# Optimization experiments

Measured on AMD Instinct MI355X. Metric: run time of the kernel, lower is better.

## Reference

```python
import jax, jax.numpy as jnp
import numpy as np

EPS = 1e-5

def _bn(x, g, b):
    m = x.mean(axis=0)
    v = x.var(axis=0)  # biased, matches torch BN training normalization
    return g * (x - m) * jax.lax.rsqrt(v + EPS) + b

def _mlp(x, W1, b1, g1, be1, W2, b2, g2, be2):
    h = jax.nn.relu(_bn(x @ W1 + b1, g1, be1))
    return jax.nn.relu(_bn(h @ W2 + b2, g2, be2))

def setup_inputs() -> dict:
    key = jax.random.key(0)
    ks = jax.random.split(key, 12)
    n, e, d, de = 100000, 1600000, 128, 16
    def lin(k, fan_in, fan_out):
        bound = 1.0 / np.sqrt(fan_in)
        k1, k2 = jax.random.split(k)
        W = jax.random.uniform(k1, (fan_in, fan_out), jnp.float32, -bound, bound)
        b = jax.random.uniform(k2, (fan_out,), jnp.float32, -bound, bound)
        return W, b
    msg_W1, msg_b1 = lin(ks[0], 2 * d + de, d)
    msg_W2, msg_b2 = lin(ks[1], d, d)
    upd_W1, upd_b1 = lin(ks[2], 3 * d, d)
    upd_W2, upd_b2 = lin(ks[3], d, d)
    return {
        "h": jax.random.normal(ks[4], (n, d), jnp.float32),
        "edge_index": jax.random.randint(ks[5], (2, e), 0, n, jnp.int64),
        "edge_attr": jax.random.normal(ks[6], (e, de), jnp.float32),
        "msg_W1": msg_W1, "msg_b1": msg_b1,
        "msg_g1": jnp.ones((d,)), "msg_be1": jnp.zeros((d,)),
        "msg_W2": msg_W2, "msg_b2": msg_b2,
        "msg_g2": jnp.ones((d,)), "msg_be2": jnp.zeros((d,)),
        "upd_W1": upd_W1, "upd_b1": upd_b1,
        "upd_g1": jnp.ones((d,)), "upd_be1": jnp.zeros((d,)),
        "upd_W2": upd_W2, "upd_b2": upd_b2,
        "upd_g2": jnp.ones((d,)), "upd_be2": jnp.zeros((d,)),
    }

def reference(h, edge_index, edge_attr,
              msg_W1, msg_b1, msg_g1, msg_be1, msg_W2, msg_b2, msg_g2, msg_be2,
              upd_W1, upd_b1, upd_g1, upd_be1, upd_W2, upd_b2, upd_g2, upd_be2):
    alpha = 0.5
    n = h.shape[0]
    src = edge_index[0]
    dst = edge_index[1]
    h_i = h[src]  # (e, d)
    h_j = h[dst]  # (e, d)
    msg_args = (msg_W1, msg_b1, msg_g1, msg_be1, msg_W2, msg_b2, msg_g2, msg_be2)
    m_st = _mlp(jnp.concatenate([h_i, h_j, edge_attr], axis=-1), *msg_args)
    m_ts = _mlp(jnp.concatenate([h_j, h_i, edge_attr], axis=-1), *msg_args)
    # NOTE: original code scatters both directions by source nodes (faithful)
    a_st = jax.ops.segment_sum(m_st, src, num_segments=n)
    a_ts = jax.ops.segment_sum(m_ts, src, num_segments=n)
    upd_in = jnp.concatenate([h, alpha * a_st, (1.0 - alpha) * a_ts], axis=-1)
    return _mlp(upd_in, upd_W1, upd_b1, upd_g1, upd_be1, upd_W2, upd_b2, upd_g2, upd_be2)
```

## Files before the change

kernel.cpp:

```cpp
#include <hip/hip_runtime.h>

#define EPS_BN 1e-5f

typedef __bf16 bf16x8 __attribute__((ext_vector_type(8)));
typedef float f32x4 __attribute__((ext_vector_type(4)));
typedef unsigned short us8 __attribute__((ext_vector_type(8)));
typedef unsigned short us4 __attribute__((ext_vector_type(4)));
typedef unsigned int u32x4 __attribute__((ext_vector_type(4)));

__device__ __forceinline__ unsigned short f2bf(float x) {
  unsigned u = __builtin_bit_cast(unsigned, x);
  unsigned r = (u + 0x7fffu + ((u >> 16) & 1u)) >> 16;
  return (unsigned short)r;
}
__device__ __forceinline__ unsigned pack2bf(float a, float b) {
  return (unsigned)f2bf(a) | ((unsigned)f2bf(b) << 16);
}
__device__ __forceinline__ unsigned long long pack4bf(float a, float b, float c, float d) {
  return (unsigned long long)pack2bf(a, b) | ((unsigned long long)pack2bf(c, d) << 32);
}
__device__ __forceinline__ float ubf(unsigned short u) {
  return __builtin_bit_cast(float, (unsigned)u << 16);
}

__device__ __forceinline__ int fragidx(int k, int c) {
  int nf = c >> 4, lr = c & 15, ks = k >> 5, lq = (k >> 3) & 3, j = k & 7;
  return ((((nf << 2) + ks) << 6) | (lq << 4) | lr) * 8 + j;
}

__global__ __launch_bounds__(256) void prep_all(
    const float* __restrict__ mW1, const float* __restrict__ mW2,
    const float* __restrict__ uW1, const float* __restrict__ uW2,
    unsigned short* __restrict__ wfrag) {
  int b = blockIdx.x;
  if (b == 7) {
    const float* s7 = mW1 + 256 * 128;
    unsigned short* oc = wfrag + 7L * 16384;
    for (int i = threadIdx.x; i < 2048; i += 256) oc[i] = f2bf(s7[i]);
    return;
  }
  const float* src;
  float sc = 1.f;
  switch (b) {
    case 0: src = mW1; break;
    case 1: src = mW1 + 16384; break;
    case 2: src = mW2; break;
    case 3: src = uW1; break;
    case 4: src = uW1 + 16384; sc = 0.5f; break;
    case 5: src = uW1 + 32768; sc = 0.5f; break;
    default: src = uW2; break;
  }
  unsigned short* oc = wfrag + (long)b * 16384;
  for (int i = threadIdx.x; i < 16384; i += 256) {
    oc[fragidx(i >> 7, i & 127)] = f2bf(src[i] * sc);
  }
}

__global__ __launch_bounds__(256) void hist_kernel(
    const int* __restrict__ SRC, long E, int* __restrict__ counts) {
  long i = (long)blockIdx.x * 256 + threadIdx.x;
  long str = (long)gridDim.x * 256;
  for (; i < E; i += str) atomicAdd(&counts[SRC[i]], 1);
}

__global__ __launch_bounds__(256) void scan1(
    const int* __restrict__ counts, int n, int* __restrict__ tmp,
    int* __restrict__ bsum) {
  __shared__ int sd[256];
  int b = blockIdx.x, tid = threadIdx.x;
  int base = b * 1024 + tid * 4;
  int c[4], t = 0;
  #pragma unroll
  for (int j = 0; j < 4; ++j) {
    int idx = base + j;
    c[j] = (idx < n) ? counts[idx] : 0;
    t += c[j];
  }
  sd[tid] = t;
  __syncthreads();
  for (int off = 1; off < 256; off <<= 1) {
    int v = (tid >= off) ? sd[tid - off] : 0;
    __syncthreads();
    sd[tid] += v;
    __syncthreads();
  }
  int run = sd[tid] - t;
  #pragma unroll
  for (int j = 0; j < 4; ++j) {
    int idx = base + j;
    if (idx < n) tmp[idx] = run;
    run += c[j];
  }
  if (tid == 255) bsum[b] = sd[255];
}

__global__ __launch_bounds__(256) void scan2(int* __restrict__ bsum, int nb) {
  __shared__ int sd[256];
  int tid = threadIdx.x;
  int v = (tid < nb) ? bsum[tid] : 0;
  sd[tid] = v;
  __syncthreads();
  for (int off = 1; off < 256; off <<= 1) {
    int x = (tid >= off) ? sd[tid - off] : 0;
    __syncthreads();
    sd[tid] += x;
    __syncthreads();
  }
  if (tid < nb) bsum[tid] = sd[tid] - v;
}

__global__ __launch_bounds__(256) void scan3(
    const int* __restrict__ tmp, const int* __restrict__ bsum, int n,
    int* __restrict__ cursor) {
  int i = blockIdx.x * 256 + threadIdx.x;
  if (i < n) cursor[i] = tmp[i] + bsum[i >> 10];
}

__global__ __launch_bounds__(256) void permute_edges(
    const int* __restrict__ SRC, const int* __restrict__ DST,
    const float* __restrict__ EA, long E, int* __restrict__ cursor,
    int* __restrict__ sS, int* __restrict__ sD,
    unsigned short* __restrict__ EAb) {
  long i = (long)blockIdx.x * 256 + threadIdx.x;
  long str = (long)gridDim.x * 256;
  for (; i < E; i += str) {
    int s = SRC[i];
    int pos = atomicAdd(&cursor[s], 1);
    sS[pos] = s;
    sD[pos] = DST[i];
    const float4* ep = (const float4*)(EA + i * 16);
    float4 a = ep[0], b = ep[1], c = ep[2], d = ep[3];
    u32x4 lo, hi;
    lo[0] = pack2bf(a.x, a.y); lo[1] = pack2bf(a.z, a.w);
    lo[2] = pack2bf(b.x, b.y); lo[3] = pack2bf(b.z, b.w);
    hi[0] = pack2bf(c.x, c.y); hi[1] = pack2bf(c.z, c.w);
    hi[2] = pack2bf(d.x, d.y); hi[3] = pack2bf(d.z, d.w);
    *(u32x4*)(EAb + (long)pos * 16) = lo;
    *(u32x4*)(EAb + (long)pos * 16 + 8) = hi;
  }
}

__global__ __launch_bounds__(256) void node_mfma_pq(
    const float* __restrict__ h, const unsigned short* __restrict__ WfA,
    unsigned short* __restrict__ pqb, int n) {
  __shared__ unsigned short WT[16384];
  int tid = threadIdx.x;
  int lid = tid & 63, w = tid >> 6, lr = lid & 15, lq = lid >> 4;
  long rbase = (long)blockIdx.x * 64 + 16 * w;
  long r = rbase + lr;
  bool rv = (r < n);
  long rl = rv ? r : 0;
  const us8* WF8 = (const us8*)WT;

  bf16x8 af[4];
  const float* Ar = h + rl * 128;
  #pragma unroll
  for (int ks = 0; ks < 4; ++ks) {
    int e0 = 32 * ks + 8 * lq;
    float4 x = *(const float4*)(Ar + e0);
    float4 y = *(const float4*)(Ar + e0 + 4);
    u32x4 t;
    t[0] = pack2bf(x.x, x.y); t[1] = pack2bf(x.z, x.w);
    t[2] = pack2bf(y.x, y.y); t[3] = pack2bf(y.z, y.w);
    if (!rv) { t[0] = 0; t[1] = 0; t[2] = 0; t[3] = 0; }
    af[ks] = __builtin_bit_cast(bf16x8, t);
  }

  f32x4 accP[8], accQ[8];
  #pragma unroll
  for (int nf = 0; nf < 8; ++nf) {
    accP[nf] = f32x4{0.f, 0.f, 0.f, 0.f};
    accQ[nf] = f32x4{0.f, 0.f, 0.f, 0.f};
  }

  for (int i = tid; i < 2048; i += 256) ((us8*)WT)[i] = ((const us8*)WfA)[i];
  __syncthreads();
  #pragma unroll
  for (int nf = 0; nf < 8; ++nf) {
    #pragma unroll
    for (int ks = 0; ks < 4; ++ks) {
      bf16x8 bf = __builtin_bit_cast(bf16x8, WF8[(nf * 4 + ks) * 64 + lid]);
      accP[nf] = __builtin_amdgcn_mfma_f32_16x16x32_bf16(af[ks], bf, accP[nf], 0, 0, 0);
    }
  }
  __syncthreads();
  for (int i = tid; i < 2048; i += 256) ((us8*)WT)[i] = ((const us8*)(WfA + 16384))[i];
  __syncthreads();
  #pragma unroll
  for (int nf = 0; nf < 8; ++nf) {
    #pragma unroll
    for (int ks = 0; ks < 4; ++ks) {
      bf16x8 bf = __builtin_bit_cast(bf16x8, WF8[(nf * 4 + ks) * 64 + lid]);
      accQ[nf] = __builtin_amdgcn_mfma_f32_16x16x32_bf16(af[ks], bf, accQ[nf], 0, 0, 0);
    }
  }

  #pragma unroll
  for (int nf = 0; nf < 8; ++nf) {
    #pragma unroll
    for (int i = 0; i < 4; ++i) {
      long nd = rbase + 4 * lq + i;
      if (nd < n) {
        int ch = 16 * nf + lr;
        pqb[nd * 256 + ch] = f2bf(accP[nf][i]);
        pqb[nd * 256 + 128 + ch] = f2bf(accQ[nf][i]);
      }
    }
  }
}

template <bool ABF16>
__global__ __launch_bounds__(256) void node_mfma(
    const void* A0, const void* A1, const void* A2,
    const unsigned short* __restrict__ Wf,
    float* __restrict__ C, int n, int dostats,
    float* __restrict__ sum_out, float* __restrict__ ssq_out, int nk) {
  __shared__ unsigned short WT[16384];
  int tid = threadIdx.x;
  int lid = tid & 63, w = tid >> 6, lr = lid & 15, lq = lid >> 4;
  long rbase = (long)blockIdx.x * 64 + 16 * w;

  const void* As[3] = {A0, A1, A2};
  f32x4 acc[8];
  #pragma unroll
  for (int nf = 0; nf < 8; ++nf) acc[nf] = f32x4{0.f, 0.f, 0.f, 0.f};

  long r = rbase + lr;
  bool rv = (r < n);
  long rl = rv ? r : 0;
  const us8* WF8 = (const us8*)WT;

  for (int c = 0; c < nk; ++c) {
    if (c) __syncthreads();
    const us8* src = (const us8*)(Wf + (long)c * 16384);
    for (int i = tid; i < 2048; i += 256) ((us8*)WT)[i] = src[i];
    __syncthreads();

    bf16x8 af[4];
    if (ABF16) {
      const us8* Ar = (const us8*)((const unsigned short*)As[c] + rl * 128);
      #pragma unroll
      for (int ks = 0; ks < 4; ++ks) {
        us8 v = Ar[ks * 4 + lq];
        if (!rv) v = us8{0, 0, 0, 0, 0, 0, 0, 0};
        af[ks] = __builtin_bit_cast(bf16x8, v);
      }
    } else {
      const float* Ar = (const float*)As[c] + rl * 128;
      #pragma unroll
      for (int ks = 0; ks < 4; ++ks) {
        int e0 = 32 * ks + 8 * lq;
        float4 x = *(const float4*)(Ar + e0);
        float4 y = *(const float4*)(Ar + e0 + 4);
        u32x4 t;
        t[0] = pack2bf(x.x, x.y); t[1] = pack2bf(x.z, x.w);
        t[2] = pack2bf(y.x, y.y); t[3] = pack2bf(y.z, y.w);
        if (!rv) { t[0] = 0; t[1] = 0; t[2] = 0; t[3] = 0; }
        af[ks] = __builtin_bit_cast(bf16x8, t);
      }
    }
    #pragma unroll
    for (int nf = 0; nf < 8; ++nf) {
      #pragma unroll
      for (int ks = 0; ks < 4; ++ks) {
        bf16x8 bf = __builtin_bit_cast(bf16x8, WF8[(nf * 4 + ks) * 64 + lid]);
        acc[nf] = __builtin_amdgcn_mfma_f32_16x16x32_bf16(af[ks], bf, acc[nf], 0, 0, 0);
      }
    }
  }

  float lsum[8], lssq[8];
  #pragma unroll
  for (int nf = 0; nf < 8; ++nf) { lsum[nf] = 0.f; lssq[nf] = 0.f; }
  #pragma unroll
  for (int nf = 0; nf < 8; ++nf) {
    #pragma unroll
    for (int i = 0; i < 4; ++i) {
      long nd = rbase + 4 * lq + i;
      if (nd < n) {
        float v = acc[nf][i];
        C[nd * 128 + 16 * nf + lr] = v;
        lsum[nf] += v; lssq[nf] += v * v;
      }
    }
  }
  if (dostats) {
    #pragma unroll
    for (int nf = 0; nf < 8; ++nf) {
      float v0 = lsum[nf]; v0 += __shfl_xor(v0, 16); v0 += __shfl_xor(v0, 32);
      float v1 = lssq[nf]; v1 += __shfl_xor(v1, 16); v1 += __shfl_xor(v1, 32);
      if (lq == 0) {
        atomicAdd(&sum_out[16 * nf + lr], v0);
        atomicAdd(&ssq_out[16 * nf + lr], v1);
      }
    }
  }
}

__global__ __launch_bounds__(256) void msg_stats1b(
    const unsigned short* __restrict__ PQ,
    const unsigned short* __restrict__ EAb, const float* __restrict__ W1e,
    const int* __restrict__ SRC, const int* __restrict__ DST, long E,
    float* __restrict__ stats) {
  __shared__ float Wel[16][128];
  __shared__ float red[32][16];
  int tid = threadIdx.x;
  for (int i = tid; i < 16 * 128; i += 256) ((float*)Wel)[i] = W1e[i];
  for (int i = tid; i < 512; i += 256) ((float*)red)[i] = 0.f;
  __syncthreads();
  int c4 = tid & 31, grp = tid >> 5;
  float4 s_st = {0,0,0,0}, q_st = {0,0,0,0}, s_ts = {0,0,0,0}, q_ts = {0,0,0,0};
  long stride = (long)gridDim.x * 8;
  for (long e = (long)blockIdx.x * 8 + grp; e < E; e += stride) {
    int s = SRC[e], t = DST[e];
    const unsigned short* Rs = PQ + (long)s * 256;
    const unsigned short* Rt = PQ + (long)t * 256;
    us4 Ps = *(const us4*)(Rs + 4 * c4);
    us4 Qs = *(const us4*)(Rs + 128 + 4 * c4);
    us4 Pt = *(const us4*)(Rt + 4 * c4);
    us4 Qt = *(const us4*)(Rt + 128 + 4 * c4);
    us8 evlo = *(const us8*)(EAb + e * 16);
    us8 evhi = *(const us8*)(EAb + e * 16 + 8);
    float rx = 0.f, ry = 0.f, rz = 0.f, rw = 0.f;
    #pragma unroll
    for (int k = 0; k < 16; ++k) {
      float f = (k < 8) ? ubf(evlo[k & 7]) : ubf(evhi[k & 7]);
      const float4 w4 = *(const float4*)&Wel[k][c4 * 4];
      rx = fmaf(f, w4.x, rx); ry = fmaf(f, w4.y, ry);
      rz = fmaf(f, w4.z, rz); rw = fmaf(f, w4.w, rw);
    }
    float zx = ubf(Ps[0]) + ubf(Qt[0]) + rx, zy = ubf(Ps[1]) + ubf(Qt[1]) + ry;
    float zz = ubf(Ps[2]) + ubf(Qt[2]) + rz, zw = ubf(Ps[3]) + ubf(Qt[3]) + rw;
    s_st.x += zx; s_st.y += zy; s_st.z += zz; s_st.w += zw;
    q_st.x += zx * zx; q_st.y += zy * zy; q_st.z += zz * zz; q_st.w += zw * zw;
    float ux = ubf(Pt[0]) + ubf(Qs[0]) + rx, uy = ubf(Pt[1]) + ubf(Qs[1]) + ry;
    float uz = ubf(Pt[2]) + ubf(Qs[2]) + rz, uw = ubf(Pt[3]) + ubf(Qs[3]) + rw;
    s_ts.x += ux; s_ts.y += uy; s_ts.z += uz; s_ts.w += uw;
    q_ts.x += ux * ux; q_ts.y += uy * uy; q_ts.z += uz * uz; q_ts.w += uw * uw;
  }
  atomicAdd(&red[c4][0], s_st.x);  atomicAdd(&red[c4][1], s_st.y);
  atomicAdd(&red[c4][2], s_st.z);  atomicAdd(&red[c4][3], s_st.w);
  atomicAdd(&red[c4][4], q_st.x);  atomicAdd(&red[c4][5], q_st.y);
  atomicAdd(&red[c4][6], q_st.z);  atomicAdd(&red[c4][7], q_st.w);
  atomicAdd(&red[c4][8], s_ts.x);  atomicAdd(&red[c4][9], s_ts.y);
  atomicAdd(&red[c4][10], s_ts.z); atomicAdd(&red[c4][11], s_ts.w);
  atomicAdd(&red[c4][12], q_ts.x); atomicAdd(&red[c4][13], q_ts.y);
  atomicAdd(&red[c4][14], q_ts.z); atomicAdd(&red[c4][15], q_ts.w);
  __syncthreads();
  #pragma unroll
  for (int rep = 0; rep < 2; ++rep) {
    int j = rep * 256 + tid;
    int cc = j >> 4, k = j & 15, group = k >> 2, comp = k & 3;
    atomicAdd(&stats[group * 128 + cc * 4 + comp], red[cc][k]);
  }
}

template <bool SCATTER>
__global__ __launch_bounds__(256) void msg_mfma6(
    const unsigned short* __restrict__ PQ,
    const unsigned short* __restrict__ EAb,
    const unsigned short* __restrict__ Web,
    const unsigned short* __restrict__ W2f,
    const int* __restrict__ SRC, const int* __restrict__ DST, long E,
    const float* __restrict__ sc1, const float* __restrict__ sc2,
    float* __restrict__ stats2,
    float* __restrict__ a_st, float* __restrict__ a_ts) {
  __shared__ unsigned short W2F[16384];
  __shared__ unsigned short Atile[2][32][136];
  __shared__ int sArr[32];

  int tid = threadIdx.x;
  int c4 = tid & 31;
  int slot = tid >> 5;
  int lid = tid & 63, w = tid >> 6, lr = lid & 15, lq = lid >> 4;
  int dir = w >> 1;
  int half = (w & 1) * 16;

  for (int i = tid; i < 2048; i += 256) ((us8*)W2F)[i] = ((const us8*)W2f)[i];
  const us8* W2F8 = (const us8*)W2F;

  us4 wreg[16];
  #pragma unroll
  for (int k = 0; k < 16; ++k) wreg[k] = *(const us4*)(Web + k * 128 + c4 * 4);

  const float4* sc1v = (const float4*)sc1;
  float4 scst = sc1v[c4], shst = sc1v[32 + c4];
  float4 scts = sc1v[64 + c4], shts = sc1v[96 + c4];

  float s2[8], h2[8];
  float ssum[8], sssq[8];
  if constexpr (SCATTER) {
    const float* scd = sc2 + dir * 256;
    #pragma unroll
    for (int nf = 0; nf < 8; ++nf) {
      int ch = 16 * nf + lr;
      s2[nf] = scd[ch]; h2[nf] = scd[128 + ch];
    }
  } else {
    #pragma unroll
    for (int nf = 0; nf < 8; ++nf) { ssum[nf] = 0.f; sssq[nf] = 0.f; }
  }
  float* accOut = dir ? a_ts : a_st;
  __syncthreads();

  for (long tb = (long)blockIdx.x * 32; tb < E; tb += (long)gridDim.x * 32) {
    int nE = (int)(E - tb < 32 ? E - tb : 32);

    #pragma unroll
    for (int rep = 0; rep < 4; ++rep) {
      int er = rep * 8 + slot;
      if (er < nE) {
        long e = tb + er;
        int s = SRC[e], t = DST[e];
        if (SCATTER && c4 == 0) sArr[er] = s;
        const us4* Rs = (const us4*)(PQ + (long)s * 256);
        const us4* Rt = (const us4*)(PQ + (long)t * 256);
        us4 Ps = Rs[c4];
        us4 Qs = Rs[32 + c4];
        us4 Pt = Rt[c4];
        us4 Qt = Rt[32 + c4];
        us8 evlo = *(const us8*)(EAb + e * 16);
        us8 evhi = *(const us8*)(EAb + e * 16 + 8);
        float rx = 0.f, ry = 0.f, rz = 0.f, rw = 0.f;
        #pragma unroll
        for (int k = 0; k < 16; ++k) {
          float f = (k < 8) ? ubf(evlo[k & 7]) : ubf(evhi[k & 7]);
          rx = fmaf(f, ubf(wreg[k][0]), rx);
          ry = fmaf(f, ubf(wreg[k][1]), ry);
          rz = fmaf(f, ubf(wreg[k][2]), rz);
          rw = fmaf(f, ubf(wreg[k][3]), rw);
        }
        float ax = fmaxf(fmaf(ubf(Ps[0]) + ubf(Qt[0]) + rx, scst.x, shst.x), 0.f);
        float ay = fmaxf(fmaf(ubf(Ps[1]) + ubf(Qt[1]) + ry, scst.y, shst.y), 0.f);
        float az = fmaxf(fmaf(ubf(Ps[2]) + ubf(Qt[2]) + rz, scst.z, shst.z), 0.f);
        float aw = fmaxf(fmaf(ubf(Ps[3]) + ubf(Qt[3]) + rw, scst.w, shst.w), 0.f);
        *(unsigned long long*)&Atile[0][er][c4 * 4] = pack4bf(ax, ay, az, aw);
        float bx = fmaxf(fmaf(ubf(Pt[0]) + ubf(Qs[0]) + rx, scts.x, shts.x), 0.f);
        float by = fmaxf(fmaf(ubf(Pt[1]) + ubf(Qs[1]) + ry, scts.y, shts.y), 0.f);
        float bz = fmaxf(fmaf(ubf(Pt[2]) + ubf(Qs[2]) + rz, scts.z, shts.z), 0.f);
        float bw = fmaxf(fmaf(ubf(Pt[3]) + ubf(Qs[3]) + rw, scts.w, shts.w), 0.f);
        *(unsigned long long*)&Atile[1][er][c4 * 4] = pack4bf(bx, by, bz, bw);
      } else {
        *(unsigned long long*)&Atile[0][er][c4 * 4] = 0ull;
        *(unsigned long long*)&Atile[1][er][c4 * 4] = 0ull;
      }
    }
    __syncthreads();

    int arow = half + lr;
    const char* ap = (const char*)&Atile[dir][arow][0];
    int acolb = lq * 16;
    bf16x8 af[4];
    #pragma unroll
    for (int ks = 0; ks < 4; ++ks) {
      af[ks] = *(const bf16x8*)(ap + ks * 64 + acolb);
    }
    int srow[4];
    if constexpr (SCATTER) {
      #pragma unroll
      for (int i = 0; i < 4; ++i) {
        int row = half + 4 * lq + i;
        srow[i] = (row < nE) ? sArr[row] : -1;
      }
    }
    #pragma unroll
    for (int nf = 0; nf < 8; ++nf) {
      f32x4 acc = {0.f, 0.f, 0.f, 0.f};
      #pragma unroll
      for (int ks = 0; ks < 4; ++ks) {
        bf16x8 bf = __builtin_bit_cast(bf16x8, W2F8[(nf * 4 + ks) * 64 + lid]);
        acc = __builtin_amdgcn_mfma_f32_16x16x32_bf16(af[ks], bf, acc, 0, 0, 0);
      }
      if constexpr (SCATTER) {
        int ch = 16 * nf + lr;
        int cur = srow[0];
        float m = fmaxf(fmaf(acc[0], s2[nf], h2[nf]), 0.f);
        #pragma unroll
        for (int i = 1; i < 4; ++i) {
          float v = fmaxf(fmaf(acc[i], s2[nf], h2[nf]), 0.f);
          if (srow[i] == cur) {
            m += v;
          } else {
            if (cur >= 0 && m != 0.f) atomicAdd(&accOut[(long)cur * 128 + ch], m);
            cur = srow[i]; m = v;
          }
        }
        if (cur >= 0 && m != 0.f) atomicAdd(&accOut[(long)cur * 128 + ch], m);
      } else {
        #pragma unroll
        for (int i = 0; i < 4; ++i) {
          ssum[nf] += acc[i]; sssq[nf] += acc[i] * acc[i];
        }
      }
    }
    __syncthreads();
  }

  if constexpr (!SCATTER) {
    #pragma unroll
    for (int nf = 0; nf < 8; ++nf) {
      float v0 = ssum[nf]; v0 += __shfl_xor(v0, 16); v0 += __shfl_xor(v0, 32);
      float v1 = sssq[nf]; v1 += __shfl_xor(v1, 16); v1 += __shfl_xor(v1, 32);
      if (lq == 0) {
        int ch = 16 * nf + lr;
        atomicAdd(&stats2[dir * 256 + ch], v0);
        atomicAdd(&stats2[dir * 256 + 128 + ch], v1);
      }
    }
  }
}

__global__ void bn_finalize(const float* __restrict__ sum, const float* __restrict__ ssq,
                            float invN, const float* __restrict__ g,
                            const float* __restrict__ be,
                            float* __restrict__ sc, float* __restrict__ sh) {
  int j = threadIdx.x;
  float m = sum[j] * invN;
  float v = ssq[j] * invN - m * m;
  float s = g[j] * rsqrtf(v + EPS_BN);
  sc[j] = s;
  sh[j] = be[j] - m * s;
}

__global__ __launch_bounds__(256) void prescale_relu(
    const float* __restrict__ X, const float* __restrict__ scsh,
    unsigned* __restrict__ out, long nrows) {
  long gid = (long)blockIdx.x * 256 + threadIdx.x;
  int c2 = (int)(gid & 63);
  float s0 = scsh[2 * c2], s1 = scsh[2 * c2 + 1];
  float h0 = scsh[128 + 2 * c2], h1 = scsh[128 + 2 * c2 + 1];
  const float2* X2 = (const float2*)X;
  long rstride = ((long)gridDim.x * 256) >> 6;
  for (long row = gid >> 6; row < nrows; row += rstride) {
    float2 x = X2[row * 64 + c2];
    out[row * 64 + c2] = pack2bf(fmaxf(fmaf(x.x, s0, h0), 0.f),
                                 fmaxf(fmaf(x.y, s1, h1), 0.f));
  }
}

__global__ __launch_bounds__(256) void bn_relu_out(
    const float* __restrict__ U2, const float* __restrict__ scsh,
    float* __restrict__ out, long total) {
  long i = (long)blockIdx.x * blockDim.x + threadIdx.x;
  long stride = (long)gridDim.x * blockDim.x;
  for (; i < total; i += stride) {
    int j = (int)(i & 127);
    out[i] = fmaxf(fmaf(U2[i], scsh[j], scsh[128 + j]), 0.f);
  }
}

extern "C" void kernel_launch(void* const* d_in, const int* in_sizes, int n_in,
                              void* d_out, int out_size, void* d_ws, size_t ws_size,
                              hipStream_t stream) {
  const float* h    = (const float*)d_in[0];
  const int*   ei   = (const int*)d_in[1];
  const float* ea   = (const float*)d_in[2];
  const float* mW1  = (const float*)d_in[3];
  const float* mg1  = (const float*)d_in[5];
  const float* mbe1 = (const float*)d_in[6];
  const float* mW2  = (const float*)d_in[7];
  const float* mg2  = (const float*)d_in[9];
  const float* mbe2 = (const float*)d_in[10];
  const float* uW1  = (const float*)d_in[11];
  const float* ug1  = (const float*)d_in[13];
  const float* ube1 = (const float*)d_in[14];
  const float* uW2  = (const float*)d_in[15];
  const float* ug2  = (const float*)d_in[17];
  const float* ube2 = (const float*)d_in[18];

  int n = in_sizes[0] / 128;
  long E = (long)(in_sizes[1] / 2);
  const int* SRC = ei;
  const int* DST = ei + E;
  const float* W1e = mW1 + 256 * 128;

  size_t nf = (size_t)n * 128;
  unsigned short* pqb = (unsigned short*)d_ws;
  float* a_st = (float*)(pqb + (size_t)n * 256);
  float* a_ts = a_st + nf;
  float* st   = a_ts + nf;
  unsigned short* wfrag = (unsigned short*)(st + 3072);
  unsigned short* wfA  = wfrag;
  unsigned short* wfW2 = wfrag + 2 * 16384;
  unsigned short* wfU1 = wfrag + 3 * 16384;
  unsigned short* wfU2 = wfrag + 6 * 16384;
  unsigned short* wfWe = wfrag + 7 * 16384;
  int* sS = (int*)(wfWe + 2048);
  int* sD = sS + E;
  unsigned short* EAb = (unsigned short*)(sD + E);
  int* counts = (int*)(EAb + (size_t)E * 16);
  int* tmp = counts + n;
  int* bsum = tmp + n;

  float invE = 1.0f / (float)E;
  float invN = 1.0f / (float)n;
  int nblk = (n + 63) / 64;
  int nb1 = (n + 1023) / 1024;

  prep_all<<<8, 256, 0, stream>>>(mW1, mW2, uW1, uW2, wfrag);
  hipMemsetAsync(st, 0, 3072 * sizeof(float), stream);
  hipMemsetAsync(a_st, 0, 2 * nf * sizeof(float), stream);
  hipMemsetAsync(counts, 0, (size_t)n * sizeof(int), stream);

  hist_kernel<<<1024, 256, 0, stream>>>(SRC, E, counts);
  scan1<<<nb1, 256, 0, stream>>>(counts, n, tmp, bsum);
  scan2<<<1, 256, 0, stream>>>(bsum, nb1);
  scan3<<<(n + 255) / 256, 256, 0, stream>>>(tmp, bsum, n, counts);
  permute_edges<<<1024, 256, 0, stream>>>(SRC, DST, ea, E, counts, sS, sD, EAb);

  node_mfma_pq<<<nblk, 256, 0, stream>>>(h, wfA, pqb, n);

  msg_stats1b<<<2048, 256, 0, stream>>>(pqb, EAb, W1e, sS, sD, E, st);
  bn_finalize<<<1, 128, 0, stream>>>(st + 0,   st + 128, invE, mg1, mbe1, st + 1536, st + 1664);
  bn_finalize<<<1, 128, 0, stream>>>(st + 256, st + 384, invE, mg1, mbe1, st + 1792, st + 1920);

  msg_mfma6<false><<<1536, 256, 0, stream>>>(
      pqb, EAb, wfWe, wfW2, sS, sD, E, st + 1536, nullptr, st + 512, nullptr, nullptr);
  bn_finalize<<<1, 128, 0, stream>>>(st + 512, st + 640, invE, mg2, mbe2, st + 2048, st + 2176);
  bn_finalize<<<1, 128, 0, stream>>>(st + 768, st + 896, invE, mg2, mbe2, st + 2304, st + 2432);

  msg_mfma6<true><<<1536, 256, 0, stream>>>(
      pqb, EAb, wfWe, wfW2, sS, sD, E, st + 1536, st + 2048, nullptr, a_st, a_ts);

  float* u1 = (float*)pqb;
  node_mfma<false><<<nblk, 256, 0, stream>>>(h, a_st, a_ts, wfU1,
                                             u1, n, 1, st + 1024, st + 1152, 3);
  bn_finalize<<<1, 128, 0, stream>>>(st + 1024, st + 1152, invN, ug1, ube1, st + 2560, st + 2688);

  unsigned short* u1p = (unsigned short*)a_st;
  float* u2 = a_ts;
  prescale_relu<<<2048, 256, 0, stream>>>(u1, st + 2560, (unsigned*)u1p, n);
  node_mfma<true><<<nblk, 256, 0, stream>>>(u1p, nullptr, nullptr, wfU2,
                                            u2, n, 1, st + 1280, st + 1408, 1);
  bn_finalize<<<1, 128, 0, stream>>>(st + 1280, st + 1408, invN, ug2, ube2, st + 2816, st + 2944);

  bn_relu_out<<<2048, 256, 0, stream>>>(u2, st + 2816, (float*)d_out, (long)n * 128);
}
```

Before: 2.567 ms.

## Double-buffer edge tile build and add uniform-source scatter fast path

The message kernel now keeps two shared-memory A tiles and sArr buffers. It builds the next tile's gathered first-layer activations while running the MFMA on the current tile, which removes one barrier per iteration and lets the gathers overlap compute. In the scatter variant, when all 16 rows of a wave's half-tile share one source node (edges are sorted by source), it reduces across lanes with shuffles and issues a single atomic per channel instead of up to four. The cost is roughly doubled LDS per block (about 50 KB), which may lower occupancy, plus some extra register pressure.

```diff
diff --git a/kernel.cpp b/kernel.cpp
--- a/kernel.cpp
+++ b/kernel.cpp
@@ -356,7 +356,7 @@
 }
 
 template <bool SCATTER>
-__global__ __launch_bounds__(256) void msg_mfma6(
+__global__ __launch_bounds__(256) void msg_mfma8(
     const unsigned short* __restrict__ PQ,
     const unsigned short* __restrict__ EAb,
     const unsigned short* __restrict__ Web,
@@ -366,8 +366,8 @@
     float* __restrict__ stats2,
     float* __restrict__ a_st, float* __restrict__ a_ts) {
   __shared__ unsigned short W2F[16384];
-  __shared__ unsigned short Atile[2][32][136];
-  __shared__ int sArr[32];
+  __shared__ unsigned short Atile[2][2][32][136];
+  __shared__ int sArr[2][32];
 
   int tid = threadIdx.x;
   int c4 = tid & 31;
@@ -401,18 +401,19 @@
     for (int nf = 0; nf < 8; ++nf) { ssum[nf] = 0.f; sssq[nf] = 0.f; }
   }
   float* accOut = dir ? a_ts : a_st;
-  __syncthreads();
-
-  for (long tb = (long)blockIdx.x * 32; tb < E; tb += (long)gridDim.x * 32) {
+
+  long tb0 = (long)blockIdx.x * 32;
+  long tstep = (long)gridDim.x * 32;
+
+  auto phaseA = [&](long tb, int p) {
     int nE = (int)(E - tb < 32 ? E - tb : 32);
-
     #pragma unroll
     for (int rep = 0; rep < 4; ++rep) {
       int er = rep * 8 + slot;
       if (er < nE) {
         long e = tb + er;
         int s = SRC[e], t = DST[e];
-        if (SCATTER && c4 == 0) sArr[er] = s;
+        if (SCATTER && c4 == 0) sArr[p][er] = s;
         const us4* Rs = (const us4*)(PQ + (long)s * 256);
         const us4* Rt = (const us4*)(PQ + (long)t * 256);
         us4 Ps = Rs[c4];
@@ -434,21 +435,31 @@
         float ay = fmaxf(fmaf(ubf(Ps[1]) + ubf(Qt[1]) + ry, scst.y, shst.y), 0.f);
         float az = fmaxf(fmaf(ubf(Ps[2]) + ubf(Qt[2]) + rz, scst.z, shst.z), 0.f);
         float aw = fmaxf(fmaf(ubf(Ps[3]) + ubf(Qt[3]) + rw, scst.w, shst.w), 0.f);
-        *(unsigned long long*)&Atile[0][er][c4 * 4] = pack4bf(ax, ay, az, aw);
+        *(unsigned long long*)&Atile[p][0][er][c4 * 4] = pack4bf(ax, ay, az, aw);
         float bx = fmaxf(fmaf(ubf(Pt[0]) + ubf(Qs[0]) + rx, scts.x, shts.x), 0.f);
         float by = fmaxf(fmaf(ubf(Pt[1]) + ubf(Qs[1]) + ry, scts.y, shts.y), 0.f);
         float bz = fmaxf(fmaf(ubf(Pt[2]) + ubf(Qs[2]) + rz, scts.z, shts.z), 0.f);
         float bw = fmaxf(fmaf(ubf(Pt[3]) + ubf(Qs[3]) + rw, scts.w, shts.w), 0.f);
-        *(unsigned long long*)&Atile[1][er][c4 * 4] = pack4bf(bx, by, bz, bw);
+        *(unsigned long long*)&Atile[p][1][er][c4 * 4] = pack4bf(bx, by, bz, bw);
       } else {
-        *(unsigned long long*)&Atile[0][er][c4 * 4] = 0ull;
-        *(unsigned long long*)&Atile[1][er][c4 * 4] = 0ull;
-      }
-    }
-    __syncthreads();
+        *(unsigned long long*)&Atile[p][0][er][c4 * 4] = 0ull;
+        *(unsigned long long*)&Atile[p][1][er][c4 * 4] = 0ull;
+      }
+    }
+  };
+
+  if (tb0 < E) phaseA(tb0, 0);
+  __syncthreads();
+
+  int p = 0;
+  for (long tb = tb0; tb < E; tb += tstep) {
+    int nE = (int)(E - tb < 32 ? E - tb : 32);
+    long tnext = tb + tstep;
+
+    if (tnext < E) phaseA(tnext, p ^ 1);
 
     int arow = half + lr;
-    const char* ap = (const char*)&Atile[dir][arow][0];
+    const char* ap = (const char*)&Atile[p][dir][arow][0];
     int acolb = lq * 16;
     bf16x8 af[4];
     #pragma unroll
@@ -456,11 +467,17 @@
       af[ks] = *(const bf16x8*)(ap + ks * 64 + acolb);
     }
     int srow[4];
+    bool uniform = false;
+    int usrc = -1;
     if constexpr (SCATTER) {
       #pragma unroll
       for (int i = 0; i < 4; ++i) {
         int row = half + 4 * lq + i;
-        srow[i] = (row < nE) ? sArr[row] : -1;
+        srow[i] = (row < nE) ? sArr[p][row] : -1;
+      }
+      if (half + 15 < nE) {
+        usrc = sArr[p][half];
+        uniform = (usrc == sArr[p][half + 15]);
       }
     }
     #pragma unroll
@@ -473,19 +490,30 @@
       }
       if constexpr (SCATTER) {
         int ch = 16 * nf + lr;
-        int cur = srow[0];
-        float m = fmaxf(fmaf(acc[0], s2[nf], h2[nf]), 0.f);
-        #pragma unroll
-        for (int i = 1; i < 4; ++i) {
-          float v = fmaxf(fmaf(acc[i], s2[nf], h2[nf]), 0.f);
-          if (srow[i] == cur) {
-            m += v;
-          } else {
-            if (cur >= 0 && m != 0.f) atomicAdd(&accOut[(long)cur * 128 + ch], m);
-            cur = srow[i]; m = v;
+        if (uniform) {
+          float m = 0.f;
+          #pragma unroll
+          for (int i = 0; i < 4; ++i)
+            m += fmaxf(fmaf(acc[i], s2[nf], h2[nf]), 0.f);
+          m += __shfl_xor(m, 16);
+          m += __shfl_xor(m, 32);
+          if (lq == 0 && m != 0.f)
+            atomicAdd(&accOut[(long)usrc * 128 + ch], m);
+        } else {
+          int cur = srow[0];
+          float m = fmaxf(fmaf(acc[0], s2[nf], h2[nf]), 0.f);
+          #pragma unroll
+          for (int i = 1; i < 4; ++i) {
+            float v = fmaxf(fmaf(acc[i], s2[nf], h2[nf]), 0.f);
+            if (srow[i] == cur) {
+              m += v;
+            } else {
+              if (cur >= 0 && m != 0.f) atomicAdd(&accOut[(long)cur * 128 + ch], m);
+              cur = srow[i]; m = v;
+            }
           }
+          if (cur >= 0 && m != 0.f) atomicAdd(&accOut[(long)cur * 128 + ch], m);
         }
-        if (cur >= 0 && m != 0.f) atomicAdd(&accOut[(long)cur * 128 + ch], m);
       } else {
         #pragma unroll
         for (int i = 0; i < 4; ++i) {
@@ -494,6 +522,7 @@
       }
     }
     __syncthreads();
+    p ^= 1;
   }
 
   if constexpr (!SCATTER) {
@@ -614,12 +643,12 @@
   bn_finalize<<<1, 128, 0, stream>>>(st + 0,   st + 128, invE, mg1, mbe1, st + 1536, st + 1664);
   bn_finalize<<<1, 128, 0, stream>>>(st + 256, st + 384, invE, mg1, mbe1, st + 1792, st + 1920);
 
-  msg_mfma6<false><<<1536, 256, 0, stream>>>(
+  msg_mfma8<false><<<1536, 256, 0, stream>>>(
       pqb, EAb, wfWe, wfW2, sS, sD, E, st + 1536, nullptr, st + 512, nullptr, nullptr);
   bn_finalize<<<1, 128, 0, stream>>>(st + 512, st + 640, invE, mg2, mbe2, st + 2048, st + 2176);
   bn_finalize<<<1, 128, 0, stream>>>(st + 768, st + 896, invE, mg2, mbe2, st + 2304, st + 2432);
 
-  msg_mfma6<true><<<1536, 256, 0, stream>>>(
+  msg_mfma8<true><<<1536, 256, 0, stream>>>(
       pqb, EAb, wfWe, wfW2, sS, sD, E, st + 1536, st + 2048, nullptr, a_st, a_ts);
 
   float* u1 = (float*)pqb;
```

Measured after the change: 2.470 ms. 3.8% less time.
